# Performance work log

Hardware: AMD Instinct MI355X
Metric: run time of the kernel (lower is better)

## Reference

```python
import jax, jax.numpy as jnp
import numpy as np

B, T, D = 4, 2048, 2048
P, K, ALPHA, R = 512, 16, 4, 32
E_RATIO = 0.8
EPS = 1e-6


def rmsnorm(x, g):
    return x * jax.lax.rsqrt(jnp.mean(x * x, axis=-1, keepdims=True) + EPS) * g


def dale_signs():
    # first e_ratio*P neurons excitatory (+1), rest inhibitory (-1)
    return jnp.where(jnp.arange(P) < int(E_RATIO * P), 1.0, -1.0)


def quant_dale(w, signs):
    # STE sign-quantization with per-neuron mean-abs scale + Dale's-law sign constraint
    scale = jnp.mean(jnp.abs(w), axis=-1, keepdims=True)  # [P,1]
    q = scale * signs[:, None] * jnp.ones_like(w)         # magnitude=scale, sign fixed per neuron
    return w + jax.lax.stop_gradient(q - w)


def synapse_graph(x, idx, w):
    # x: [B,T,D], idx: [P,K] int, w: [P,K] -> dendritic inputs [B,T,P,K]
    return jnp.take(x, idx, axis=-1) * w


def perceptron(x_dend, Wp, Wout, signs):
    Wq = quant_dale(Wp, signs)                              # [P,K]
    u = jnp.einsum('btpk,pk->btp', x_dend, Wq)              # [B,T,P]
    f = jax.nn.sigmoid(u)                                   # gate [B,T,P]
    f_out = quant_dale(Wout, signs)                         # [P,ALPHA]
    y = (f * u)[..., None] * f_out                          # [B,T,P,ALPHA]
    return u, f, y, f_out


def low_rank_ssm(t, f, s0, U, V, Wgate, bgate):
    # t,f: [B,T,P]; s0: [B,R]. Low-rank gated linear scan in R dims.
    z = jnp.einsum('btp,pr->btr', t, U)
    lam = jax.nn.sigmoid(jnp.einsum('btp,pr->btr', f, Wgate) + bgate)

    def step(s, inp):
        z_t, l_t = inp
        s = l_t * s + z_t
        return s, s

    sT, S = jax.lax.scan(step, s0, (jnp.moveaxis(z, 1, 0), jnp.moveaxis(lam, 1, 0)))
    tilde = jnp.einsum('btr,rp->btp', jnp.moveaxis(S, 0, 1), V)
    return tilde, sT


def flatten_ports(y):
    return y.reshape(*y.shape[:-2], P * ALPHA)


def setup_inputs() -> dict:
    key = jax.random.key(0)
    ks = jax.random.split(key, 14)
    sc = 0.1
    return {
        'x': jax.random.normal(ks[0], (B, T, D), jnp.float32),
        'state': jnp.zeros((B, R), jnp.float32),
        'g1': jnp.ones((D,), jnp.float32),
        'g2': jnp.ones((D,), jnp.float32),
        'idx_ssm': jax.random.randint(ks[1], (P, K), 0, D),
        'wg_ssm': jax.random.normal(ks[2], (P, K), jnp.float32) * sc,
        'idx_mlp': jax.random.randint(ks[3], (P, K), 0, D),
        'wg_mlp': jax.random.normal(ks[4], (P, K), jnp.float32) * sc,
        'Wp_ssm': jax.random.normal(ks[5], (P, K), jnp.float32) * sc,
        'Wout_ssm': jax.random.normal(ks[6], (P, ALPHA), jnp.float32) * sc,
        'Wp_mlp': jax.random.normal(ks[7], (P, K), jnp.float32) * sc,
        'Wout_mlp': jax.random.normal(ks[8], (P, ALPHA), jnp.float32) * sc,
        'U': jax.random.normal(ks[9], (P, R), jnp.float32) * sc,
        'V': jax.random.normal(ks[10], (R, P), jnp.float32) * sc,
        'Wgate': jax.random.normal(ks[11], (P, R), jnp.float32) * sc,
        'bgate': jnp.zeros((R,), jnp.float32),
    }


def reference(x, state, g1, g2, idx_ssm, wg_ssm, idx_mlp, wg_mlp,
              Wp_ssm, Wout_ssm, Wp_mlp, Wout_mlp, U, V, Wgate, bgate):
    signs = dale_signs()
    # --- SSM branch ---
    h1 = rmsnorm(x, g1)
    x_dend_ssm = synapse_graph(h1, idx_ssm, wg_ssm)
    u_ssm, f_ssm, _, f_out = perceptron(x_dend_ssm, Wp_ssm, Wout_ssm, signs)
    t_ssm = f_ssm * u_ssm
    tilde_t, new_state = low_rank_ssm(t_ssm, f_ssm, state, U, V, Wgate, bgate)
    y_ssm = (f_ssm * tilde_t)[..., None] * f_out            # [B,T,P,ALPHA]
    x_after = x + flatten_ports(y_ssm)
    # --- MLP branch ---
    h2 = rmsnorm(x_after, g2)
    x_dend_mlp = synapse_graph(h2, idx_mlp, wg_mlp)
    _, _, y_mlp, _ = perceptron(x_dend_mlp, Wp_mlp, Wout_mlp, signs)
    x_out = x_after + flatten_ports(y_mlp)
    return x_out, new_state
```

## Files before the change

kernel.cpp:

```cpp
#include <hip/hip_runtime.h>
#include <hip/hip_bf16.h>

#define B_ 4
#define T_ 2048
#define D_ 2048
#define P_ 512
#define K_ 16
#define ALPHA_ 4
#define R_ 32
#define NE_ 409
#define EPS_ 1e-6f
#define G_ 4

typedef unsigned short u16;
typedef unsigned int u32;
typedef _Float16 h2t __attribute__((ext_vector_type(2)));

__device__ __forceinline__ float sigmoidf_(float x) {
  return 1.0f / (1.0f + __expf(-x));
}
__device__ __forceinline__ u16 f2bfb(float f) {
  __hip_bfloat16 h = __float2bfloat16(f);
  return *reinterpret_cast<u16*>(&h);
}
__device__ __forceinline__ float bflo(u32 u) { return __uint_as_float(u << 16); }
__device__ __forceinline__ float bfhi(u32 u) { return __uint_as_float(u & 0xFFFF0000u); }
__device__ __forceinline__ u32 packbf(float lo, float hi) {
  return ((u32)f2bfb(hi) << 16) | (u32)f2bfb(lo);
}
__device__ __forceinline__ u32 packh(float lo, float hi) {
#if __has_builtin(__builtin_amdgcn_cvt_pkrtz)
  return __builtin_bit_cast(u32, __builtin_amdgcn_cvt_pkrtz(lo, hi));
#else
  union { _Float16 h; u16 u; } a, b;
  a.h = (_Float16)lo; b.h = (_Float16)hi;
  return ((u32)b.u << 16) | a.u;
#endif
}
__device__ __forceinline__ u32 duph(float w) {
  union { _Float16 h; u16 u; } c;
  c.h = (_Float16)w;
  return ((u32)c.u << 16) | c.u;
}
__device__ __forceinline__ h2t pkfma(u32 h, u32 w, h2t acc) {
  return __builtin_bit_cast(h2t, h) * __builtin_bit_cast(h2t, w) + acc;
}

__global__ void k_scalars(const float* __restrict__ Wp_s, const float* __restrict__ Wo_s,
                          const float* __restrict__ Wp_m, const float* __restrict__ Wo_m,
                          float* __restrict__ wq_s, float* __restrict__ fo_s,
                          float* __restrict__ wq_m, float* __restrict__ fo_m) {
  int p = blockIdx.x * blockDim.x + threadIdx.x;
  if (p >= P_) return;
  float sgn = (p < NE_) ? 1.0f : -1.0f;
  float a = 0, b = 0, c = 0, d = 0;
#pragma unroll
  for (int k = 0; k < K_; k++) {
    a += fabsf(Wp_s[p * K_ + k]);
    c += fabsf(Wp_m[p * K_ + k]);
  }
#pragma unroll
  for (int k = 0; k < ALPHA_; k++) {
    b += fabsf(Wo_s[p * ALPHA_ + k]);
    d += fabsf(Wo_m[p * ALPHA_ + k]);
  }
  wq_s[p] = sgn * a * (1.0f / K_);
  fo_s[p] = sgn * b * (1.0f / ALPHA_);
  wq_m[p] = sgn * c * (1.0f / K_);
  fo_m[p] = sgn * d * (1.0f / ALPHA_);
}

__global__ __launch_bounds__(256) void k_phase1(
    const float* __restrict__ x, const float* __restrict__ g1,
    const int* __restrict__ idx, const float* __restrict__ wg,
    const float* __restrict__ U, const float* __restrict__ Wgt,
    const float* __restrict__ bg, const float* __restrict__ wq,
    u16* __restrict__ f_ssm, float* __restrict__ z, float* __restrict__ lam) {
  __shared__ union SU {
    u32 h1p[2][D_];
    struct { float zp[G_][R_][4]; float lp[G_][R_][4]; } c;
  } su;
  __shared__ u32 tf[G_][P_];
  __shared__ float red[G_][4];

  int tid = threadIdx.x;
  int token0 = blockIdx.x * G_;
  int b = token0 >> 11;
  int t0 = token0 & (T_ - 1);

  float gv[8];
  {
    const float4* gp = reinterpret_cast<const float4*>(g1 + tid * 8);
    *reinterpret_cast<float4*>(&gv[0]) = gp[0];
    *reinterpret_cast<float4*>(&gv[4]) = gp[1];
  }
#pragma unroll
  for (int pr = 0; pr < 2; pr++) {
    int ta = 2 * pr, tb = ta + 1;
    float xv0[8], xv1[8];
    const float4* xp0 = reinterpret_cast<const float4*>(x + (size_t)(token0 + ta) * D_ + tid * 8);
    const float4* xp1 = reinterpret_cast<const float4*>(x + (size_t)(token0 + tb) * D_ + tid * 8);
    *reinterpret_cast<float4*>(&xv0[0]) = xp0[0];
    *reinterpret_cast<float4*>(&xv0[4]) = xp0[1];
    *reinterpret_cast<float4*>(&xv1[0]) = xp1[0];
    *reinterpret_cast<float4*>(&xv1[4]) = xp1[1];
    float ss0 = 0, ss1 = 0;
    u32 tmp[8];
#pragma unroll
    for (int i = 0; i < 8; i++) {
      ss0 += xv0[i] * xv0[i];
      ss1 += xv1[i] * xv1[i];
      tmp[i] = packh(xv0[i] * gv[i], xv1[i] * gv[i]);
    }
    uint4* hp = reinterpret_cast<uint4*>(&su.h1p[pr][tid * 8]);
    hp[0] = *reinterpret_cast<const uint4*>(&tmp[0]);
    hp[1] = *reinterpret_cast<const uint4*>(&tmp[4]);
#pragma unroll
    for (int off = 32; off; off >>= 1) {
      ss0 += __shfl_down(ss0, off);
      ss1 += __shfl_down(ss1, off);
    }
    if ((tid & 63) == 0) { red[ta][tid >> 6] = ss0; red[tb][tid >> 6] = ss1; }
  }
  __syncthreads();

  float inv[G_];
#pragma unroll
  for (int tok = 0; tok < G_; tok++)
    inv[tok] = rsqrtf((red[tok][0] + red[tok][1] + red[tok][2] + red[tok][3]) * (1.0f / D_) + EPS_);

#pragma unroll
  for (int j = 0; j < 2; j++) {
    int p = tid + j * 256;
    union { int4 v[4]; int s[16]; } iu;
    const int4* ip = reinterpret_cast<const int4*>(idx + p * K_);
    iu.v[0] = ip[0]; iu.v[1] = ip[1]; iu.v[2] = ip[2]; iu.v[3] = ip[3];
    u32 wd[16];
    {
      const float4* wp = reinterpret_cast<const float4*>(wg + p * K_);
#pragma unroll
      for (int q = 0; q < 4; q++) {
        float4 w = wp[q];
        wd[4 * q + 0] = duph(w.x);
        wd[4 * q + 1] = duph(w.y);
        wd[4 * q + 2] = duph(w.z);
        wd[4 * q + 3] = duph(w.w);
      }
    }
    float wqp = wq[p];
#pragma unroll
    for (int pr = 0; pr < 2; pr++) {
      int ta = 2 * pr, tb = ta + 1;
      h2t acc = {(_Float16)0.0f, (_Float16)0.0f};
#pragma unroll
      for (int k = 0; k < K_; k++) acc = pkfma(su.h1p[pr][iu.s[k]], wd[k], acc);
      float a0 = (float)acc.x, a1 = (float)acc.y;
      float u0 = wqp * inv[ta] * a0, u1 = wqp * inv[tb] * a1;
      float f0 = sigmoidf_(u0), f1 = sigmoidf_(u1);
      tf[ta][p] = packbf(f0 * u0, f0);
      tf[tb][p] = packbf(f1 * u1, f1);
      f_ssm[(size_t)(token0 + ta) * P_ + p] = f2bfb(f0);
      f_ssm[(size_t)(token0 + tb) * P_ + p] = f2bfb(f1);
    }
  }
  __syncthreads();

  int r = tid & 31, g = tid >> 5;
  float zs[G_], ls[G_];
#pragma unroll
  for (int tok = 0; tok < G_; tok++) { zs[tok] = 0; ls[tok] = 0; }
  int pb = g * 64;
#pragma unroll 2
  for (int pq = 0; pq < 16; pq++) {
    int p = pb + pq * 4;
    float u0 = U[(p + 0) * R_ + r], u1 = U[(p + 1) * R_ + r];
    float u2 = U[(p + 2) * R_ + r], u3 = U[(p + 3) * R_ + r];
    float w0 = Wgt[(p + 0) * R_ + r], w1 = Wgt[(p + 1) * R_ + r];
    float w2 = Wgt[(p + 2) * R_ + r], w3 = Wgt[(p + 3) * R_ + r];
#pragma unroll
    for (int tok = 0; tok < G_; tok++) {
      uint4 q = *reinterpret_cast<const uint4*>(&tf[tok][p]);
      zs[tok] += bflo(q.x) * u0 + bflo(q.y) * u1 + bflo(q.z) * u2 + bflo(q.w) * u3;
      ls[tok] += bfhi(q.x) * w0 + bfhi(q.y) * w1 + bfhi(q.z) * w2 + bfhi(q.w) * w3;
    }
  }
#pragma unroll
  for (int tok = 0; tok < G_; tok++) {
    zs[tok] += __shfl_down(zs[tok], 32);
    ls[tok] += __shfl_down(ls[tok], 32);
  }
  int wid = tid >> 6;
  if ((tid & 63) < 32) {
#pragma unroll
    for (int tok = 0; tok < G_; tok++) { su.c.zp[tok][r][wid] = zs[tok]; su.c.lp[tok][r][wid] = ls[tok]; }
  }
  __syncthreads();
  if (tid < R_) {
    float bgr = bg[tid];
    float z4[G_], l4[G_];
#pragma unroll
    for (int tok = 0; tok < G_; tok++) {
      float zz = su.c.zp[tok][tid][0] + su.c.zp[tok][tid][1] + su.c.zp[tok][tid][2] + su.c.zp[tok][tid][3];
      float ll = su.c.lp[tok][tid][0] + su.c.lp[tok][tid][1] + su.c.lp[tok][tid][2] + su.c.lp[tok][tid][3];
      z4[tok] = zz;
      l4[tok] = sigmoidf_(ll + bgr);
    }
    size_t o = ((size_t)(b * R_ + tid)) * T_ + t0;
    *reinterpret_cast<float4*>(&z[o]) = *reinterpret_cast<const float4*>(z4);
    *reinterpret_cast<float4*>(&lam[o]) = *reinterpret_cast<const float4*>(l4);
  }
}

__global__ __launch_bounds__(64) void k_scan(
    const float* __restrict__ z, const float* __restrict__ lam,
    const float* __restrict__ state, float* __restrict__ S,
    float* __restrict__ out_state) {
  int br = blockIdx.x;
  int lane = threadIdx.x;
  const float* zr = z + (size_t)br * T_ + lane * 32;
  const float* lr = lam + (size_t)br * T_ + lane * 32;
  float zb[32], lb[32];
#pragma unroll
  for (int i = 0; i < 32; i += 4) {
    *reinterpret_cast<float4*>(&zb[i]) = *reinterpret_cast<const float4*>(&zr[i]);
    *reinterpret_cast<float4*>(&lb[i]) = *reinterpret_cast<const float4*>(&lr[i]);
  }
  float A = 1.0f, Z = 0.0f;
#pragma unroll
  for (int i = 0; i < 32; i++) { Z = lb[i] * Z + zb[i]; A *= lb[i]; }
  for (int off = 1; off < 64; off <<= 1) {
    float Ap = __shfl_up(A, off);
    float Zp = __shfl_up(Z, off);
    if (lane >= off) { Z = A * Zp + Z; A = A * Ap; }
  }
  float s0 = state[br];
  float Ae = __shfl_up(A, 1);
  float Ze = __shfl_up(Z, 1);
  float s = (lane == 0) ? s0 : (Ae * s0 + Ze);
  float sb[32];
#pragma unroll
  for (int i = 0; i < 32; i++) { s = lb[i] * s + zb[i]; sb[i] = s; }
  float* Sr = S + (size_t)br * T_ + lane * 32;
#pragma unroll
  for (int i = 0; i < 32; i += 4)
    *reinterpret_cast<float4*>(&Sr[i]) = *reinterpret_cast<const float4*>(&sb[i]);
  if (lane == 63) out_state[br] = s;
}

__global__ __launch_bounds__(256) void k_phase3(
    const float* __restrict__ x, const float* __restrict__ g2,
    const int* __restrict__ idx, const float* __restrict__ wg,
    const float* __restrict__ V, const float* __restrict__ S,
    const u16* __restrict__ f_ssm, const float* __restrict__ fo_s,
    const float* __restrict__ wq_m, const float* __restrict__ fo_m,
    float* __restrict__ out) {
  __shared__ float Sl[G_][R_];
  __shared__ u32 h2p[2][D_];
  __shared__ float red[G_][4];

  int tid = threadIdx.x;
  int token0 = blockIdx.x * G_;
  int b = token0 >> 11;
  int t0 = token0 & (T_ - 1);
  int p0 = 2 * tid;

  if (tid < G_ * R_) {
    int tok = tid >> 5, r = tid & 31;
    Sl[tok][r] = S[((size_t)(b * R_ + r)) * T_ + t0 + tok];
  }
  __syncthreads();

  float til0[G_], til1[G_];
#pragma unroll
  for (int tok = 0; tok < G_; tok++) { til0[tok] = 0; til1[tok] = 0; }
#pragma unroll 4
  for (int r = 0; r < R_; r++) {
    float2 vv = *reinterpret_cast<const float2*>(V + r * P_ + p0);
#pragma unroll
    for (int tok = 0; tok < G_; tok++) {
      float s = Sl[tok][r];
      til0[tok] += s * vv.x;
      til1[tok] += s * vv.y;
    }
  }

  float2 fo = *reinterpret_cast<const float2*>(fo_s + p0);
  float gv[8];
  {
    const float4* gp = reinterpret_cast<const float4*>(g2 + tid * 8);
    *reinterpret_cast<float4*>(&gv[0]) = gp[0];
    *reinterpret_cast<float4*>(&gv[4]) = gp[1];
  }

  float xa[G_][8];
#pragma unroll
  for (int pr = 0; pr < 2; pr++) {
    int ta = 2 * pr, tb = ta + 1;
#pragma unroll
    for (int h = 0; h < 2; h++) {
      int tok = ta + h;
      u32 ff = *reinterpret_cast<const u32*>(f_ssm + (size_t)(token0 + tok) * P_ + p0);
      float val0 = bflo(ff) * (h ? til0[tb] : til0[ta]) * fo.x;
      float val1 = bfhi(ff) * (h ? til1[tb] : til1[ta]) * fo.y;
      float xv[8];
      const float4* xp = reinterpret_cast<const float4*>(x + (size_t)(token0 + tok) * D_ + tid * 8);
      *reinterpret_cast<float4*>(&xv[0]) = xp[0];
      *reinterpret_cast<float4*>(&xv[4]) = xp[1];
      float ss = 0;
#pragma unroll
      for (int a = 0; a < 4; a++) {
        float v0 = xv[a] + val0;
        float v1 = xv[4 + a] + val1;
        xa[tok][a] = v0;
        xa[tok][4 + a] = v1;
        ss += v0 * v0 + v1 * v1;
      }
#pragma unroll
      for (int off = 32; off; off >>= 1) ss += __shfl_down(ss, off);
      if ((tid & 63) == 0) red[tok][tid >> 6] = ss;
    }
    u32 tmp[8];
#pragma unroll
    for (int i = 0; i < 8; i++)
      tmp[i] = packh(xa[ta][i] * gv[i], xa[tb][i] * gv[i]);
    uint4* hp = reinterpret_cast<uint4*>(&h2p[pr][tid * 8]);
    hp[0] = *reinterpret_cast<const uint4*>(&tmp[0]);
    hp[1] = *reinterpret_cast<const uint4*>(&tmp[4]);
  }
  __syncthreads();

  union { int4 v[4]; int s[16]; } iu0, iu1;
  u32 wd0[16], wd1[16];
  {
    const int4* ip0 = reinterpret_cast<const int4*>(idx + p0 * K_);
    const int4* ip1 = reinterpret_cast<const int4*>(idx + (p0 + 1) * K_);
#pragma unroll
    for (int q = 0; q < 4; q++) { iu0.v[q] = ip0[q]; iu1.v[q] = ip1[q]; }
    const float4* wp0 = reinterpret_cast<const float4*>(wg + p0 * K_);
    const float4* wp1 = reinterpret_cast<const float4*>(wg + (p0 + 1) * K_);
#pragma unroll
    for (int q = 0; q < 4; q++) {
      float4 w0 = wp0[q], w1 = wp1[q];
      wd0[4 * q + 0] = duph(w0.x); wd0[4 * q + 1] = duph(w0.y);
      wd0[4 * q + 2] = duph(w0.z); wd0[4 * q + 3] = duph(w0.w);
      wd1[4 * q + 0] = duph(w1.x); wd1[4 * q + 1] = duph(w1.y);
      wd1[4 * q + 2] = duph(w1.z); wd1[4 * q + 3] = duph(w1.w);
    }
  }
  float2 wqm = *reinterpret_cast<const float2*>(wq_m + p0);
  float2 fom = *reinterpret_cast<const float2*>(fo_m + p0);

#pragma unroll
  for (int pr = 0; pr < 2; pr++) {
    h2t acc0 = {(_Float16)0.0f, (_Float16)0.0f};
    h2t acc1 = {(_Float16)0.0f, (_Float16)0.0f};
#pragma unroll
    for (int k = 0; k < K_; k++) {
      acc0 = pkfma(h2p[pr][iu0.s[k]], wd0[k], acc0);
      acc1 = pkfma(h2p[pr][iu1.s[k]], wd1[k], acc1);
    }
    float a00 = (float)acc0.x, a01 = (float)acc0.y;
    float a10 = (float)acc1.x, a11 = (float)acc1.y;
#pragma unroll
    for (int h = 0; h < 2; h++) {
      int tok = 2 * pr + h;
      float invt = rsqrtf((red[tok][0] + red[tok][1] + red[tok][2] + red[tok][3]) * (1.0f / D_) + EPS_);
      float accA = h ? a01 : a00;
      float accB = h ? a11 : a10;
      float u0 = wqm.x * invt * accA, u1 = wqm.y * invt * accB;
      float f0 = sigmoidf_(u0), f1 = sigmoidf_(u1);
      float val0 = f0 * u0 * fom.x, val1 = f1 * u1 * fom.y;
      float ov[8];
#pragma unroll
      for (int a = 0; a < 4; a++) {
        ov[a] = xa[tok][a] + val0;
        ov[4 + a] = xa[tok][4 + a] + val1;
      }
      float4* op = reinterpret_cast<float4*>(out + (size_t)(token0 + tok) * D_ + tid * 8);
      op[0] = *reinterpret_cast<const float4*>(&ov[0]);
      op[1] = *reinterpret_cast<const float4*>(&ov[4]);
    }
  }
}

extern "C" void kernel_launch(void* const* d_in, const int* in_sizes, int n_in,
                              void* d_out, int out_size, void* d_ws, size_t ws_size,
                              hipStream_t stream) {
  const float* x     = (const float*)d_in[0];
  const float* state = (const float*)d_in[1];
  const float* g1    = (const float*)d_in[2];
  const float* g2    = (const float*)d_in[3];
  const int*   idx_s = (const int*)d_in[4];
  const float* wg_s  = (const float*)d_in[5];
  const int*   idx_m = (const int*)d_in[6];
  const float* wg_m  = (const float*)d_in[7];
  const float* Wp_s  = (const float*)d_in[8];
  const float* Wo_s  = (const float*)d_in[9];
  const float* Wp_m  = (const float*)d_in[10];
  const float* Wo_m  = (const float*)d_in[11];
  const float* U     = (const float*)d_in[12];
  const float* V     = (const float*)d_in[13];
  const float* Wgt   = (const float*)d_in[14];
  const float* bg    = (const float*)d_in[15];
  float* out = (float*)d_out;

  char* ws = (char*)d_ws;
  float* wq_s = (float*)(ws + 0);
  float* fo_s = (float*)(ws + 2048);
  float* wq_m = (float*)(ws + 4096);
  float* fo_m = (float*)(ws + 6144);
  u16* f_ssm = (u16*)(ws + 8192);
  size_t off = 8192 + (size_t)B_ * T_ * P_ * 2;
  float* z   = (float*)(ws + off); off += (size_t)B_ * R_ * T_ * 4;
  float* lam = (float*)(ws + off); off += (size_t)B_ * R_ * T_ * 4;
  float* S   = (float*)(ws + off);

  hipLaunchKernelGGL(k_scalars, dim3(2), dim3(256), 0, stream,
                     Wp_s, Wo_s, Wp_m, Wo_m, wq_s, fo_s, wq_m, fo_m);
  hipLaunchKernelGGL(k_phase1, dim3(B_ * T_ / G_), dim3(256), 0, stream,
                     x, g1, idx_s, wg_s, U, Wgt, bg, wq_s, f_ssm, z, lam);
  hipLaunchKernelGGL(k_scan, dim3(B_ * R_), dim3(64), 0, stream,
                     z, lam, state, S, out + (size_t)B_ * T_ * D_);
  hipLaunchKernelGGL(k_phase3, dim3(B_ * T_ / G_), dim3(256), 0, stream,
                     x, g2, idx_m, wg_m, V, S, f_ssm, fo_s, wq_m, fo_m, out);
}
```

Before: 208.1 us.

## Double block size, precompute fp16 weight pairs, use packed fp16 projection

Phase1 and phase3 now run 512 threads per block, one neuron per thread, with each thread handling 4 elements of the hidden row instead of 8. The prologue kernel pre-converts U, Wgate and the synapse weights into duplicated fp16 pairs, so the main kernels no longer convert them per block. The z/lambda projection now uses packed fp16 FMAs over per-token-pair t and f values instead of fp32 math on bf16-unpacked values. This aims for more parallelism and fewer ALU instructions, at the cost of fp16 accumulation precision and more partial-sum reduction slots.

Result: no change. 207.6 us (-0.2%).

```diff
diff --git a/kernel.cpp b/kernel.cpp
--- a/kernel.cpp
+++ b/kernel.cpp
@@ -19,14 +19,12 @@
 __device__ __forceinline__ float sigmoidf_(float x) {
   return 1.0f / (1.0f + __expf(-x));
 }
+__device__ __forceinline__ float bfb2f(u16 u) {
+  return __uint_as_float(((u32)u) << 16);
+}
 __device__ __forceinline__ u16 f2bfb(float f) {
   __hip_bfloat16 h = __float2bfloat16(f);
   return *reinterpret_cast<u16*>(&h);
-}
-__device__ __forceinline__ float bflo(u32 u) { return __uint_as_float(u << 16); }
-__device__ __forceinline__ float bfhi(u32 u) { return __uint_as_float(u & 0xFFFF0000u); }
-__device__ __forceinline__ u32 packbf(float lo, float hi) {
-  return ((u32)f2bfb(hi) << 16) | (u32)f2bfb(lo);
 }
 __device__ __forceinline__ u32 packh(float lo, float hi) {
 #if __has_builtin(__builtin_amdgcn_cvt_pkrtz)
@@ -48,8 +46,12 @@
 
 __global__ void k_scalars(const float* __restrict__ Wp_s, const float* __restrict__ Wo_s,
                           const float* __restrict__ Wp_m, const float* __restrict__ Wo_m,
+                          const float* __restrict__ U, const float* __restrict__ Wgt,
+                          const float* __restrict__ wg_s, const float* __restrict__ wg_m,
                           float* __restrict__ wq_s, float* __restrict__ fo_s,
-                          float* __restrict__ wq_m, float* __restrict__ fo_m) {
+                          float* __restrict__ wq_m, float* __restrict__ fo_m,
+                          u32* __restrict__ Ud, u32* __restrict__ Wd,
+                          u32* __restrict__ wgd_s, u32* __restrict__ wgd_m) {
   int p = blockIdx.x * blockDim.x + threadIdx.x;
   if (p >= P_) return;
   float sgn = (p < NE_) ? 1.0f : -1.0f;
@@ -68,53 +70,56 @@
   fo_s[p] = sgn * b * (1.0f / ALPHA_);
   wq_m[p] = sgn * c * (1.0f / K_);
   fo_m[p] = sgn * d * (1.0f / ALPHA_);
-}
-
-__global__ __launch_bounds__(256) void k_phase1(
+#pragma unroll
+  for (int r = 0; r < R_; r++) {
+    Ud[p * R_ + r] = duph(U[p * R_ + r]);
+    Wd[p * R_ + r] = duph(Wgt[p * R_ + r]);
+  }
+#pragma unroll
+  for (int k = 0; k < K_; k++) {
+    wgd_s[p * K_ + k] = duph(wg_s[p * K_ + k]);
+    wgd_m[p * K_ + k] = duph(wg_m[p * K_ + k]);
+  }
+}
+
+__global__ __launch_bounds__(512) void k_phase1(
     const float* __restrict__ x, const float* __restrict__ g1,
-    const int* __restrict__ idx, const float* __restrict__ wg,
-    const float* __restrict__ U, const float* __restrict__ Wgt,
+    const int* __restrict__ idx, const u32* __restrict__ wgd,
+    const u32* __restrict__ Ud, const u32* __restrict__ Wd,
     const float* __restrict__ bg, const float* __restrict__ wq,
     u16* __restrict__ f_ssm, float* __restrict__ z, float* __restrict__ lam) {
   __shared__ union SU {
     u32 h1p[2][D_];
-    struct { float zp[G_][R_][4]; float lp[G_][R_][4]; } c;
+    struct { float zp[G_][R_][8]; float lp[G_][R_][8]; } c;
   } su;
-  __shared__ u32 tf[G_][P_];
-  __shared__ float red[G_][4];
+  __shared__ u32 tp[2][P_];
+  __shared__ u32 fp[2][P_];
+  __shared__ float red[G_][8];
 
   int tid = threadIdx.x;
   int token0 = blockIdx.x * G_;
   int b = token0 >> 11;
   int t0 = token0 & (T_ - 1);
 
-  float gv[8];
-  {
-    const float4* gp = reinterpret_cast<const float4*>(g1 + tid * 8);
-    *reinterpret_cast<float4*>(&gv[0]) = gp[0];
-    *reinterpret_cast<float4*>(&gv[4]) = gp[1];
-  }
+  float gv[4];
+  *reinterpret_cast<float4*>(gv) = *reinterpret_cast<const float4*>(g1 + tid * 4);
 #pragma unroll
   for (int pr = 0; pr < 2; pr++) {
     int ta = 2 * pr, tb = ta + 1;
-    float xv0[8], xv1[8];
-    const float4* xp0 = reinterpret_cast<const float4*>(x + (size_t)(token0 + ta) * D_ + tid * 8);
-    const float4* xp1 = reinterpret_cast<const float4*>(x + (size_t)(token0 + tb) * D_ + tid * 8);
-    *reinterpret_cast<float4*>(&xv0[0]) = xp0[0];
-    *reinterpret_cast<float4*>(&xv0[4]) = xp0[1];
-    *reinterpret_cast<float4*>(&xv1[0]) = xp1[0];
-    *reinterpret_cast<float4*>(&xv1[4]) = xp1[1];
+    float xv0[4], xv1[4];
+    *reinterpret_cast<float4*>(xv0) =
+        *reinterpret_cast<const float4*>(x + (size_t)(token0 + ta) * D_ + tid * 4);
+    *reinterpret_cast<float4*>(xv1) =
+        *reinterpret_cast<const float4*>(x + (size_t)(token0 + tb) * D_ + tid * 4);
     float ss0 = 0, ss1 = 0;
-    u32 tmp[8];
-#pragma unroll
-    for (int i = 0; i < 8; i++) {
+    u32 tmp[4];
+#pragma unroll
+    for (int i = 0; i < 4; i++) {
       ss0 += xv0[i] * xv0[i];
       ss1 += xv1[i] * xv1[i];
       tmp[i] = packh(xv0[i] * gv[i], xv1[i] * gv[i]);
     }
-    uint4* hp = reinterpret_cast<uint4*>(&su.h1p[pr][tid * 8]);
-    hp[0] = *reinterpret_cast<const uint4*>(&tmp[0]);
-    hp[1] = *reinterpret_cast<const uint4*>(&tmp[4]);
+    *reinterpret_cast<uint4*>(&su.h1p[pr][tid * 4]) = *reinterpret_cast<const uint4*>(tmp);
 #pragma unroll
     for (int off = 32; off; off >>= 1) {
       ss0 += __shfl_down(ss0, off);
@@ -126,39 +131,32 @@
 
   float inv[G_];
 #pragma unroll
-  for (int tok = 0; tok < G_; tok++)
-    inv[tok] = rsqrtf((red[tok][0] + red[tok][1] + red[tok][2] + red[tok][3]) * (1.0f / D_) + EPS_);
-
-#pragma unroll
-  for (int j = 0; j < 2; j++) {
-    int p = tid + j * 256;
+  for (int tok = 0; tok < G_; tok++) {
+    float s = 0;
+#pragma unroll
+    for (int w = 0; w < 8; w++) s += red[tok][w];
+    inv[tok] = rsqrtf(s * (1.0f / D_) + EPS_);
+  }
+
+  {
+    int p = tid;
     union { int4 v[4]; int s[16]; } iu;
     const int4* ip = reinterpret_cast<const int4*>(idx + p * K_);
     iu.v[0] = ip[0]; iu.v[1] = ip[1]; iu.v[2] = ip[2]; iu.v[3] = ip[3];
-    u32 wd[16];
-    {
-      const float4* wp = reinterpret_cast<const float4*>(wg + p * K_);
-#pragma unroll
-      for (int q = 0; q < 4; q++) {
-        float4 w = wp[q];
-        wd[4 * q + 0] = duph(w.x);
-        wd[4 * q + 1] = duph(w.y);
-        wd[4 * q + 2] = duph(w.z);
-        wd[4 * q + 3] = duph(w.w);
-      }
-    }
+    union { uint4 v[4]; u32 s[16]; } wd;
+    const uint4* wp = reinterpret_cast<const uint4*>(wgd + p * K_);
+    wd.v[0] = wp[0]; wd.v[1] = wp[1]; wd.v[2] = wp[2]; wd.v[3] = wp[3];
     float wqp = wq[p];
 #pragma unroll
     for (int pr = 0; pr < 2; pr++) {
       int ta = 2 * pr, tb = ta + 1;
       h2t acc = {(_Float16)0.0f, (_Float16)0.0f};
 #pragma unroll
-      for (int k = 0; k < K_; k++) acc = pkfma(su.h1p[pr][iu.s[k]], wd[k], acc);
-      float a0 = (float)acc.x, a1 = (float)acc.y;
-      float u0 = wqp * inv[ta] * a0, u1 = wqp * inv[tb] * a1;
+      for (int k = 0; k < K_; k++) acc = pkfma(su.h1p[pr][iu.s[k]], wd.s[k], acc);
+      float u0 = wqp * inv[ta] * (float)acc.x, u1 = wqp * inv[tb] * (float)acc.y;
       float f0 = sigmoidf_(u0), f1 = sigmoidf_(u1);
-      tf[ta][p] = packbf(f0 * u0, f0);
-      tf[tb][p] = packbf(f1 * u1, f1);
+      tp[pr][p] = packh(f0 * u0, f1 * u1);
+      fp[pr][p] = packh(f0, f1);
       f_ssm[(size_t)(token0 + ta) * P_ + p] = f2bfb(f0);
       f_ssm[(size_t)(token0 + tb) * P_ + p] = f2bfb(f1);
     }
@@ -166,23 +164,23 @@
   __syncthreads();
 
   int r = tid & 31, g = tid >> 5;
-  float zs[G_], ls[G_];
-#pragma unroll
-  for (int tok = 0; tok < G_; tok++) { zs[tok] = 0; ls[tok] = 0; }
-  int pb = g * 64;
-#pragma unroll 2
-  for (int pq = 0; pq < 16; pq++) {
-    int p = pb + pq * 4;
-    float u0 = U[(p + 0) * R_ + r], u1 = U[(p + 1) * R_ + r];
-    float u2 = U[(p + 2) * R_ + r], u3 = U[(p + 3) * R_ + r];
-    float w0 = Wgt[(p + 0) * R_ + r], w1 = Wgt[(p + 1) * R_ + r];
-    float w2 = Wgt[(p + 2) * R_ + r], w3 = Wgt[(p + 3) * R_ + r];
-#pragma unroll
-    for (int tok = 0; tok < G_; tok++) {
-      uint4 q = *reinterpret_cast<const uint4*>(&tf[tok][p]);
-      zs[tok] += bflo(q.x) * u0 + bflo(q.y) * u1 + bflo(q.z) * u2 + bflo(q.w) * u3;
-      ls[tok] += bfhi(q.x) * w0 + bfhi(q.y) * w1 + bfhi(q.z) * w2 + bfhi(q.w) * w3;
-    }
+  float zs[G_] = {0, 0, 0, 0}, ls[G_] = {0, 0, 0, 0};
+  int pb = g * 32;
+#pragma unroll
+  for (int c = 0; c < 4; c++) {
+    h2t z0 = {(_Float16)0.0f, (_Float16)0.0f}, z1 = z0, l0 = z0, l1 = z0;
+#pragma unroll
+    for (int i = 0; i < 8; i++) {
+      int p = pb + c * 8 + i;
+      u32 ud = Ud[p * R_ + r];
+      u32 wdd = Wd[p * R_ + r];
+      z0 = pkfma(tp[0][p], ud, z0);
+      z1 = pkfma(tp[1][p], ud, z1);
+      l0 = pkfma(fp[0][p], wdd, l0);
+      l1 = pkfma(fp[1][p], wdd, l1);
+    }
+    zs[0] += (float)z0.x; zs[1] += (float)z0.y; zs[2] += (float)z1.x; zs[3] += (float)z1.y;
+    ls[0] += (float)l0.x; ls[1] += (float)l0.y; ls[2] += (float)l1.x; ls[3] += (float)l1.y;
   }
 #pragma unroll
   for (int tok = 0; tok < G_; tok++) {
@@ -200,8 +198,9 @@
     float z4[G_], l4[G_];
 #pragma unroll
     for (int tok = 0; tok < G_; tok++) {
-      float zz = su.c.zp[tok][tid][0] + su.c.zp[tok][tid][1] + su.c.zp[tok][tid][2] + su.c.zp[tok][tid][3];
-      float ll = su.c.lp[tok][tid][0] + su.c.lp[tok][tid][1] + su.c.lp[tok][tid][2] + su.c.lp[tok][tid][3];
+      float zz = 0, ll = 0;
+#pragma unroll
+      for (int w = 0; w < 8; w++) { zz += su.c.zp[tok][tid][w]; ll += su.c.lp[tok][tid][w]; }
       z4[tok] = zz;
       l4[tok] = sigmoidf_(ll + bgr);
     }
@@ -247,22 +246,22 @@
   if (lane == 63) out_state[br] = s;
 }
 
-__global__ __launch_bounds__(256) void k_phase3(
+__global__ __launch_bounds__(512) void k_phase3(
     const float* __restrict__ x, const float* __restrict__ g2,
-    const int* __restrict__ idx, const float* __restrict__ wg,
+    const int* __restrict__ idx, const u32* __restrict__ wgd,
     const float* __restrict__ V, const float* __restrict__ S,
     const u16* __restrict__ f_ssm, const float* __restrict__ fo_s,
     const float* __restrict__ wq_m, const float* __restrict__ fo_m,
     float* __restrict__ out) {
   __shared__ float Sl[G_][R_];
   __shared__ u32 h2p[2][D_];
-  __shared__ float red[G_][4];
+  __shared__ float red[G_][8];
 
   int tid = threadIdx.x;
   int token0 = blockIdx.x * G_;
   int b = token0 >> 11;
   int t0 = token0 & (T_ - 1);
-  int p0 = 2 * tid;
+  int p = tid;
 
   if (tid < G_ * R_) {
     int tok = tid >> 5, r = tid & 31;
@@ -270,115 +269,86 @@
   }
   __syncthreads();
 
-  float til0[G_], til1[G_];
-#pragma unroll
-  for (int tok = 0; tok < G_; tok++) { til0[tok] = 0; til1[tok] = 0; }
+  float til[G_] = {0, 0, 0, 0};
 #pragma unroll 4
   for (int r = 0; r < R_; r++) {
-    float2 vv = *reinterpret_cast<const float2*>(V + r * P_ + p0);
-#pragma unroll
-    for (int tok = 0; tok < G_; tok++) {
-      float s = Sl[tok][r];
-      til0[tok] += s * vv.x;
-      til1[tok] += s * vv.y;
-    }
-  }
-
-  float2 fo = *reinterpret_cast<const float2*>(fo_s + p0);
-  float gv[8];
-  {
-    const float4* gp = reinterpret_cast<const float4*>(g2 + tid * 8);
-    *reinterpret_cast<float4*>(&gv[0]) = gp[0];
-    *reinterpret_cast<float4*>(&gv[4]) = gp[1];
-  }
-
-  float xa[G_][8];
+    float v = V[r * P_ + p];
+#pragma unroll
+    for (int tok = 0; tok < G_; tok++) til[tok] += Sl[tok][r] * v;
+  }
+
+  float fo = fo_s[p];
+  float gv[4];
+  *reinterpret_cast<float4*>(gv) = *reinterpret_cast<const float4*>(g2 + tid * 4);
+
+  float xa[G_][4];
 #pragma unroll
   for (int pr = 0; pr < 2; pr++) {
     int ta = 2 * pr, tb = ta + 1;
 #pragma unroll
     for (int h = 0; h < 2; h++) {
       int tok = ta + h;
-      u32 ff = *reinterpret_cast<const u32*>(f_ssm + (size_t)(token0 + tok) * P_ + p0);
-      float val0 = bflo(ff) * (h ? til0[tb] : til0[ta]) * fo.x;
-      float val1 = bfhi(ff) * (h ? til1[tb] : til1[ta]) * fo.y;
-      float xv[8];
-      const float4* xp = reinterpret_cast<const float4*>(x + (size_t)(token0 + tok) * D_ + tid * 8);
-      *reinterpret_cast<float4*>(&xv[0]) = xp[0];
-      *reinterpret_cast<float4*>(&xv[4]) = xp[1];
+      float fv = bfb2f(f_ssm[(size_t)(token0 + tok) * P_ + p]);
+      float val = fv * til[tok] * fo;
+      float xv[4];
+      *reinterpret_cast<float4*>(xv) =
+          *reinterpret_cast<const float4*>(x + (size_t)(token0 + tok) * D_ + tid * 4);
       float ss = 0;
 #pragma unroll
       for (int a = 0; a < 4; a++) {
-        float v0 = xv[a] + val0;
-        float v1 = xv[4 + a] + val1;
-        xa[tok][a] = v0;
-        xa[tok][4 + a] = v1;
-        ss += v0 * v0 + v1 * v1;
+        float v = xv[a] + val;
+        xa[tok][a] = v;
+        ss += v * v;
       }
 #pragma unroll
       for (int off = 32; off; off >>= 1) ss += __shfl_down(ss, off);
       if ((tid & 63) == 0) red[tok][tid >> 6] = ss;
     }
-    u32 tmp[8];
-#pragma unroll
-    for (int i = 0; i < 8; i++)
+    u32 tmp[4];
+#pragma unroll
+    for (int i = 0; i < 4; i++)
       tmp[i] = packh(xa[ta][i] * gv[i], xa[tb][i] * gv[i]);
-    uint4* hp = reinterpret_cast<uint4*>(&h2p[pr][tid * 8]);
-    hp[0] = *reinterpret_cast<const uint4*>(&tmp[0]);
-    hp[1] = *reinterpret_cast<const uint4*>(&tmp[4]);
+    *reinterpret_cast<uint4*>(&h2p[pr][tid * 4]) = *reinterpret_cast<const uint4*>(tmp);
   }
   __syncthreads();
 
-  union { int4 v[4]; int s[16]; } iu0, iu1;
-  u32 wd0[16], wd1[16];
+  float invt[G_];
+#pragma unroll
+  for (int tok = 0; tok < G_; tok++) {
+    float s = 0;
+#pragma unroll
+    for (int w = 0; w < 8; w++) s += red[tok][w];
+    invt[tok] = rsqrtf(s * (1.0f / D_) + EPS_);
+  }
+
+  union { int4 v[4]; int s[16]; } iu;
+  union { uint4 v[4]; u32 s[16]; } wd;
   {
-    const int4* ip0 = reinterpret_cast<const int4*>(idx + p0 * K_);
-    const int4* ip1 = reinterpret_cast<const int4*>(idx + (p0 + 1) * K_);
-#pragma unroll
-    for (int q = 0; q < 4; q++) { iu0.v[q] = ip0[q]; iu1.v[q] = ip1[q]; }
-    const float4* wp0 = reinterpret_cast<const float4*>(wg + p0 * K_);
-    const float4* wp1 = reinterpret_cast<const float4*>(wg + (p0 + 1) * K_);
-#pragma unroll
-    for (int q = 0; q < 4; q++) {
-      float4 w0 = wp0[q], w1 = wp1[q];
-      wd0[4 * q + 0] = duph(w0.x); wd0[4 * q + 1] = duph(w0.y);
-      wd0[4 * q + 2] = duph(w0.z); wd0[4 * q + 3] = duph(w0.w);
-      wd1[4 * q + 0] = duph(w1.x); wd1[4 * q + 1] = duph(w1.y);
-      wd1[4 * q + 2] = duph(w1.z); wd1[4 * q + 3] = duph(w1.w);
-    }
-  }
-  float2 wqm = *reinterpret_cast<const float2*>(wq_m + p0);
-  float2 fom = *reinterpret_cast<const float2*>(fo_m + p0);
+    const int4* ip = reinterpret_cast<const int4*>(idx + p * K_);
+    const uint4* wp = reinterpret_cast<const uint4*>(wgd + p * K_);
+#pragma unroll
+    for (int q = 0; q < 4; q++) { iu.v[q] = ip[q]; wd.v[q] = wp[q]; }
+  }
+  float wqm = wq_m[p];
+  float fom = fo_m[p];
 
 #pragma unroll
   for (int pr = 0; pr < 2; pr++) {
-    h2t acc0 = {(_Float16)0.0f, (_Float16)0.0f};
-    h2t acc1 = {(_Float16)0.0f, (_Float16)0.0f};
-#pragma unroll
-    for (int k = 0; k < K_; k++) {
-      acc0 = pkfma(h2p[pr][iu0.s[k]], wd0[k], acc0);
-      acc1 = pkfma(h2p[pr][iu1.s[k]], wd1[k], acc1);
-    }
-    float a00 = (float)acc0.x, a01 = (float)acc0.y;
-    float a10 = (float)acc1.x, a11 = (float)acc1.y;
+    h2t acc = {(_Float16)0.0f, (_Float16)0.0f};
+#pragma unroll
+    for (int k = 0; k < K_; k++) acc = pkfma(h2p[pr][iu.s[k]], wd.s[k], acc);
 #pragma unroll
     for (int h = 0; h < 2; h++) {
       int tok = 2 * pr + h;
-      float invt = rsqrtf((red[tok][0] + red[tok][1] + red[tok][2] + red[tok][3]) * (1.0f / D_) + EPS_);
-      float accA = h ? a01 : a00;
-      float accB = h ? a11 : a10;
-      float u0 = wqm.x * invt * accA, u1 = wqm.y * invt * accB;
-      float f0 = sigmoidf_(u0), f1 = sigmoidf_(u1);
-      float val0 = f0 * u0 * fom.x, val1 = f1 * u1 * fom.y;
-      float ov[8];
-#pragma unroll
-      for (int a = 0; a < 4; a++) {
-        ov[a] = xa[tok][a] + val0;
-        ov[4 + a] = xa[tok][4 + a] + val1;
-      }
-      float4* op = reinterpret_cast<float4*>(out + (size_t)(token0 + tok) * D_ + tid * 8);
-      op[0] = *reinterpret_cast<const float4*>(&ov[0]);
-      op[1] = *reinterpret_cast<const float4*>(&ov[4]);
+      float a = h ? (float)acc.y : (float)acc.x;
+      float u = wqm * invt[tok] * a;
+      float f = sigmoidf_(u);
+      float val = f * u * fom;
+      float ov[4];
+#pragma unroll
+      for (int a2 = 0; a2 < 4; a2++) ov[a2] = xa[tok][a2] + val;
+      *reinterpret_cast<float4*>(out + (size_t)(token0 + tok) * D_ + tid * 4) =
+          *reinterpret_cast<const float4*>(ov);
     }
   }
 }
@@ -409,18 +379,23 @@
   float* fo_s = (float*)(ws + 2048);
   float* wq_m = (float*)(ws + 4096);
   float* fo_m = (float*)(ws + 6144);
-  u16* f_ssm = (u16*)(ws + 8192);
-  size_t off = 8192 + (size_t)B_ * T_ * P_ * 2;
+  u32* Ud     = (u32*)(ws + 8192);
+  u32* Wd     = (u32*)(ws + 8192 + 65536);
+  u32* wgd_s  = (u32*)(ws + 8192 + 131072);
+  u32* wgd_m  = (u32*)(ws + 8192 + 163840);
+  size_t off = 8192 + 196608;
+  u16* f_ssm = (u16*)(ws + off); off += (size_t)B_ * T_ * P_ * 2;
   float* z   = (float*)(ws + off); off += (size_t)B_ * R_ * T_ * 4;
   float* lam = (float*)(ws + off); off += (size_t)B_ * R_ * T_ * 4;
   float* S   = (float*)(ws + off);
 
   hipLaunchKernelGGL(k_scalars, dim3(2), dim3(256), 0, stream,
-                     Wp_s, Wo_s, Wp_m, Wo_m, wq_s, fo_s, wq_m, fo_m);
-  hipLaunchKernelGGL(k_phase1, dim3(B_ * T_ / G_), dim3(256), 0, stream,
-                     x, g1, idx_s, wg_s, U, Wgt, bg, wq_s, f_ssm, z, lam);
+                     Wp_s, Wo_s, Wp_m, Wo_m, U, Wgt, wg_s, wg_m,
+                     wq_s, fo_s, wq_m, fo_m, Ud, Wd, wgd_s, wgd_m);
+  hipLaunchKernelGGL(k_phase1, dim3(B_ * T_ / G_), dim3(512), 0, stream,
+                     x, g1, idx_s, wgd_s, Ud, Wd, bg, wq_s, f_ssm, z, lam);
   hipLaunchKernelGGL(k_scan, dim3(B_ * R_), dim3(64), 0, stream,
                      z, lam, state, S, out + (size_t)B_ * T_ * D_);
-  hipLaunchKernelGGL(k_phase3, dim3(B_ * T_ / G_), dim3(256), 0, stream,
-                     x, g2, idx_m, wg_m, V, S, f_ssm, fo_s, wq_m, fo_m, out);
-}
+  hipLaunchKernelGGL(k_phase3, dim3(B_ * T_ / G_), dim3(512), 0, stream,
+                     x, g2, idx_m, wgd_m, V, S, f_ssm, fo_s, wq_m, fo_m, out);
+}
```
